# Optimization experiments

Measured on AMD Instinct MI355X. Metric: run time of the kernel, lower is better.

## Reference

```python
import jax, jax.numpy as jnp
import numpy as np

N, E = 50000, 800000
NODE_IN, EDGE_IN, H, L = 2, 2, 128, 3
EPS = 1e-5


def _lin(x, W, b):
    return x @ W + b


def setup_inputs() -> dict:
    key = jax.random.key(0)
    ks = jax.random.split(key, 24)

    def gw(k, shape):
        fan_in = shape[-2]
        return jax.random.uniform(k, shape, jnp.float32, -1.0, 1.0) / np.sqrt(fan_in)

    inp = {
        "x": jax.random.normal(ks[0], (N, NODE_IN), jnp.float32),
        "edge_attr": jax.random.normal(ks[1], (E, EDGE_IN), jnp.float32),
        "edge_index": jax.random.randint(ks[2], (2, E), 0, N, jnp.int32),
        "batch": jnp.zeros((N,), jnp.int32),
        # input MLP: [NODE_IN -> H -> H], Lin+ReLU twice
        "Win0": gw(ks[3], (NODE_IN, H)), "bin0": jnp.zeros((H,), jnp.float32),
        "Win1": gw(ks[4], (H, H)), "bin1": jnp.zeros((H,), jnp.float32),
        # per-layer (stacked over L) IGConv params
        # mlp1: [H+EDGE_IN -> H -> H], Lin+ReLU twice
        "W1a": gw(ks[5], (L, H + EDGE_IN, H)), "b1a": jnp.zeros((L, H), jnp.float32),
        "W1b": gw(ks[6], (L, H, H)), "b1b": jnp.zeros((L, H), jnp.float32),
        # mlp2: [2H -> H] Lin+ReLU, then Lin+Sigmoid [H -> H]
        "W2a": gw(ks[7], (L, 2 * H, H)), "b2a": jnp.zeros((L, H), jnp.float32),
        "W2b": gw(ks[8], (L, H, H)), "b2b": jnp.zeros((L, H), jnp.float32),
        # BatchNorm affine params per layer
        "gamma": jnp.ones((L, H), jnp.float32), "beta": jnp.zeros((L, H), jnp.float32),
        # final MLP: [H -> H] Lin+ReLU, then Lin+Sigmoid [H -> 1]
        "Wf": gw(ks[9], (H, H)), "bf": jnp.zeros((H,), jnp.float32),
        "Wo": gw(ks[10], (H, 1)), "bo": jnp.zeros((1,), jnp.float32),
    }
    return inp


def _forward(x, edge_attr, edge_index, Win0, bin0, Win1, bin1,
             W1a, b1a, W1b, b1b, W2a, b2a, W2b, b2b, gamma, beta, Wf, bf, Wo, bo):
    src, dst = edge_index[0], edge_index[1]  # PyG source->target flow
    n = x.shape[0]

    # input MLP
    h = jax.nn.relu(_lin(x, Win0, bin0))
    h = jax.nn.relu(_lin(h, Win1, bin1))

    # per-edge mean-aggregation denominator (0-degree nodes -> 0 in PyG mean)
    cnt = jax.ops.segment_sum(jnp.ones((src.shape[0],), h.dtype), dst, num_segments=n)
    denom = jnp.maximum(cnt, 1.0)[:, None]  # [N,1]

    for l in range(L):
        # message: mlp1(cat(x_j, edge_attr))
        xj = h[src]                                        # [E,H] gather
        tmp = jnp.concatenate([xj, edge_attr], axis=1)     # [E,H+EDGE_IN]
        m = jax.nn.relu(_lin(tmp, W1a[l], b1a[l]))
        m = jax.nn.relu(_lin(m, W1b[l], b1b[l]))           # [E,H]
        # mean aggregate at targets
        agg = jax.ops.segment_sum(m, dst, num_segments=n) / denom  # [N,H]
        # update: mlp2(cat(x, agg)) -> Lin+ReLU -> Lin+Sigmoid
        u = jnp.concatenate([h, agg], axis=1)
        u = jax.nn.relu(_lin(u, W2a[l], b2a[l]))
        out = jax.nn.sigmoid(_lin(u, W2b[l], b2b[l]))
        # residual + BatchNorm (training-mode batch stats, biased var)
        r = h + out
        mu = jnp.mean(r, axis=0)
        var = jnp.mean((r - mu) ** 2, axis=0)
        h = (r - mu) * jax.lax.rsqrt(var + EPS) * gamma[l] + beta[l]

    # final MLP
    f = jax.nn.relu(_lin(h, Wf, bf))
    return jax.nn.sigmoid(_lin(f, Wo, bo))  # [N,1]


def reference(x, edge_attr, edge_index, batch, Win0, bin0, Win1, bin1,
              W1a, b1a, W1b, b1b, W2a, b2a, W2b, b2b, gamma, beta, Wf, bf, Wo, bo):
    # `batch` is unused by the original forward
    return _forward(x, edge_attr, edge_index, Win0, bin0, Win1, bin1,
                    W1a, b1a, W1b, b1b, W2a, b2a, W2b, b2b, gamma, beta,
                    Wf, bf, Wo, bo)
```

## Files before the change

### kernel.cpp

```cpp
#include <hip/hip_runtime.h>
#include <hip/hip_bf16.h>

#define NN 50000
#define NE 800000
#define HD 128
#define EPSV 1e-5f
#define TE 64
#define BLK 256
#define SROW 68
#define ASTR 336
#define BSTR 272

typedef unsigned short u16;
typedef __attribute__((ext_vector_type(8))) short bf16x8;
typedef __attribute__((ext_vector_type(4))) float f32x4;
#define MFMA16 __builtin_amdgcn_mfma_f32_16x16x32_bf16

__device__ __forceinline__ float sigm(float x){ return 1.0f/(1.0f+__expf(-x)); }
__device__ __forceinline__ void atomAddF(float* p, float v){ unsafeAtomicAdd(p, v); }
__device__ __forceinline__ unsigned bfr(float x){
    unsigned u = __float_as_uint(x);
    return (u + 0x7FFFu + ((u>>16)&1u)) >> 16;
}
__device__ __forceinline__ float bf2f(unsigned u){ return __uint_as_float(u<<16); }

__global__ void zero_i_k(int* __restrict__ p, int n){
    int i = blockIdx.x*blockDim.x + threadIdx.x;
    if (i < n) p[i] = 0;
}

__global__ void zero_agg_bn_k(float4* __restrict__ agg4, int n4, float* __restrict__ bn){
    int i = blockIdx.x*blockDim.x + threadIdx.x;
    if (i < n4) agg4[i] = make_float4(0.f,0.f,0.f,0.f);
    if (i < 256) bn[i] = 0.0f;
}

__global__ void count_k(const int* __restrict__ dst, int* __restrict__ cnt){
    int e = blockIdx.x*blockDim.x + threadIdx.x;
    if (e < NE) atomicAdd(&cnt[dst[e]], 1);
}
__global__ void rdenom_k(const int* __restrict__ cnt, float* __restrict__ rd){
    int i = blockIdx.x*blockDim.x + threadIdx.x;
    if (i < NN) rd[i] = 1.0f / fmaxf((float)cnt[i], 1.0f);
}

__global__ __launch_bounds__(1024) void scan_k(const int* __restrict__ cnt, int* __restrict__ off){
    __shared__ int s[1024];
    __shared__ int carryS;
    const int tid = threadIdx.x;
    if (tid == 0) carryS = 0;
    __syncthreads();
    const int NCH = (NN + 1023) / 1024;
    for (int ch = 0; ch < NCH; ++ch){
        const int i = ch*1024 + tid;
        const int v = (i < NN) ? cnt[i] : 0;
        s[tid] = v;
        __syncthreads();
        #pragma unroll
        for (int ofs = 1; ofs < 1024; ofs <<= 1){
            int t = (tid >= ofs) ? s[tid-ofs] : 0;
            __syncthreads();
            s[tid] += t;
            __syncthreads();
        }
        const int carry = carryS;
        if (i < NN) off[i] = carry + s[tid] - v;
        __syncthreads();
        if (tid == 1023) carryS = carry + s[1023];
        __syncthreads();
    }
    if (tid == 0) off[NN] = NE;
}

__global__ void fill_k(const int* __restrict__ dst, const int* __restrict__ off,
                       int* __restrict__ fill, int* __restrict__ eidx,
                       int* __restrict__ sdst){
    int e = blockIdx.x*blockDim.x + threadIdx.x;
    if (e < NE){
        int d = dst[e];
        int pos = atomicAdd(&fill[d], 1);
        int slot = off[d] + pos;
        eidx[slot] = e;
        sdst[slot] = d;
    }
}

__global__ void wconv_k(const float* __restrict__ src, u16* __restrict__ dst,
                        int K, int KP, int H){
    int idx = blockIdx.x*blockDim.x + threadIdx.x;
    if (idx >= H*KP) return;
    const int l = blockIdx.y;
    src += (size_t)l*K*H;  dst += (size_t)l*H*KP;
    int c = idx / KP, k = idx - c*KP;
    dst[idx] = (k < K) ? (u16)bfr(src[k*H + c]) : (u16)0;
}

__device__ __forceinline__ void mv_acc(const float* sT, int krows,
        const float* __restrict__ W, int c0, int eg, float acc[4][8])
{
    const float* Wp = W + c0;
    #pragma unroll 2
    for (int k=0; k<krows; ++k) {
        const float4 sv = *(const float4*)(sT + k*SROW + eg*4);
        const float4 wa = *(const float4*)(Wp + k*HD);
        const float4 wb = *(const float4*)(Wp + k*HD + 4);
        const float s[4] = {sv.x, sv.y, sv.z, sv.w};
        const float w[8] = {wa.x,wa.y,wa.z,wa.w, wb.x,wb.y,wb.z,wb.w};
        #pragma unroll
        for (int i=0;i<4;++i)
            #pragma unroll
            for (int j=0;j<8;++j)
                acc[i][j] = fmaf(s[i], w[j], acc[i][j]);
    }
}

__device__ __forceinline__ void stage_rows(float* smem, const float* __restrict__ base,
                                           const int* rowsLDS, int tid)
{
    const int e_lo = tid>>3, kq = tid&7;
    #pragma unroll
    for (int half=0; half<2; ++half) {
        const int e = e_lo + 32*half;
        const int row = rowsLDS[e];
        const float* p = base + (size_t)row*HD + kq*4;
        #pragma unroll
        for (int q=0; q<4; ++q) {
            const float4 v = *(const float4*)(p + q*32);
            const int kb = 4*kq + 32*q;
            smem[(kb+0)*SROW + e] = v.x;
            smem[(kb+1)*SROW + e] = v.y;
            smem[(kb+2)*SROW + e] = v.z;
            smem[(kb+3)*SROW + e] = v.w;
        }
    }
}

__global__ __launch_bounds__(BLK) void input_mlp_k(
    const float* __restrict__ x,
    const float* __restrict__ W0, const float* __restrict__ b0,
    const float* __restrict__ W1, const float* __restrict__ b1,
    float* __restrict__ h, u16* __restrict__ hb)
{
    __shared__ float smem[130*SROW];
    const int tid = threadIdx.x;
    const int n0 = blockIdx.x * TE;

    #pragma unroll
    for (int it=0; it<(HD*TE)/BLK; ++it) {
        int task = it*BLK + tid;
        int e = task & (TE-1);
        int c = task >> 6;
        int n = n0 + e; if (n >= NN) n = NN-1;
        float x0 = x[n*2+0], x1 = x[n*2+1];
        smem[c*SROW + e] = fmaxf(fmaf(x0, W0[c], fmaf(x1, W0[HD+c], b0[c])), 0.0f);
    }
    __syncthreads();

    const int cg = tid & 15, eg = tid >> 4, c0 = cg*8;
    float acc[4][8];
    #pragma unroll
    for (int j=0;j<8;++j){ float bv=b1[c0+j];
        #pragma unroll
        for (int i=0;i<4;++i) acc[i][j]=bv; }
    mv_acc(smem, HD, W1, c0, eg, acc);

    #pragma unroll
    for (int i=0;i<4;++i){
        int n = n0 + eg*4 + i;
        if (n < NN) {
            float4 r0, r1;
            r0.x=fmaxf(acc[i][0],0.f); r0.y=fmaxf(acc[i][1],0.f);
            r0.z=fmaxf(acc[i][2],0.f); r0.w=fmaxf(acc[i][3],0.f);
            r1.x=fmaxf(acc[i][4],0.f); r1.y=fmaxf(acc[i][5],0.f);
            r1.z=fmaxf(acc[i][6],0.f); r1.w=fmaxf(acc[i][7],0.f);
            *(float4*)&h[(size_t)n*HD + c0]     = r0;
            *(float4*)&h[(size_t)n*HD + c0 + 4] = r1;
            uint4 pk;
            pk.x = bfr(r0.x)|(bfr(r0.y)<<16); pk.y = bfr(r0.z)|(bfr(r0.w)<<16);
            pk.z = bfr(r1.x)|(bfr(r1.y)<<16); pk.w = bfr(r1.z)|(bfr(r1.w)<<16);
            *(uint4*)&hb[(size_t)n*HD + c0] = pk;
        }
    }
}

__global__ __launch_bounds__(BLK, 4) void edge_msg_kernel(
    const u16* __restrict__ hb, const float* __restrict__ ea,
    const int* __restrict__ src, const int* __restrict__ eidx,
    const int* __restrict__ sdst, const int* __restrict__ off,
    const float* __restrict__ rd,
    const u16* __restrict__ W1aT, const float* __restrict__ b1a,
    const u16* __restrict__ W1bT, const float* __restrict__ b1b,
    float* __restrict__ agg)
{
    __shared__ char bufA[TE*ASTR];
    __shared__ char bufB[TE*BSTR];

    const int tid = threadIdx.x;
    const int lane = tid & 63;
    const int l15 = lane & 15, lhi = lane >> 4;
    const int w = tid >> 6;
    const int s0 = blockIdx.x * TE;
    const int cg = tid & 15, c0 = cg*8;
    const int myrow = tid >> 2, p = tid & 3;
    const int rowL = 16*w + l15;
    const int bl = lane >> 2;

    for (int idx = tid; idx < TE*5; idx += BLK){
        const int r = idx/5, q = idx - r*5;
        *(uint4*)(bufA + r*ASTR + 256 + q*16) = make_uint4(0u,0u,0u,0u);
    }

    {
        const int et  = eidx[s0 + rowL];
        const int sv0 = src[et];
        const int sv  = __shfl(sv0, bl);
        const int etr = __shfl(et,  bl);
        const uint4* sp = (const uint4*)(hb + (size_t)sv*HD);
        uint4* dp = (uint4*)(bufA + myrow*ASTR + p*64);
        #pragma unroll
        for (int q=0;q<4;++q) dp[q] = sp[p*4+q];
        if (p == 0){
            const float2 a = *(const float2*)&ea[(size_t)etr*2];
            *(unsigned*)(bufA + myrow*ASTR + 256) = bfr(a.x) | (bfr(a.y)<<16);
        }
    }
    __syncthreads();

    f32x4 acc1[2][4];
    #pragma unroll
    for (int cc=0; cc<2; ++cc){
        const float4 bv = *(const float4*)&b1a[(2*w+cc)*16 + lhi*4];
        #pragma unroll
        for (int te=0; te<4; ++te){
            acc1[cc][te][0]=bv.x; acc1[cc][te][1]=bv.y;
            acc1[cc][te][2]=bv.z; acc1[cc][te][3]=bv.w;
        }
    }
    #pragma unroll
    for (int kk=0; kk<5; ++kk){
        const bf16x8 a0 = *(const bf16x8*)(W1aT + ((2*w  )*16 + l15)*160 + kk*32 + lhi*8);
        const bf16x8 a1 = *(const bf16x8*)(W1aT + ((2*w+1)*16 + l15)*160 + kk*32 + lhi*8);
        #pragma unroll
        for (int te=0; te<4; ++te){
            const bf16x8 bb = *(const bf16x8*)(bufA + (te*16+l15)*ASTR + kk*64 + lhi*16);
            acc1[0][te] = MFMA16(a0, bb, acc1[0][te], 0,0,0);
            acc1[1][te] = MFMA16(a1, bb, acc1[1][te], 0,0,0);
        }
    }
    #pragma unroll
    for (int cc=0; cc<2; ++cc){
        #pragma unroll
        for (int te=0; te<4; ++te){
            uint2 pk;
            pk.x = bfr(fmaxf(acc1[cc][te][0],0.f)) | (bfr(fmaxf(acc1[cc][te][1],0.f))<<16);
            pk.y = bfr(fmaxf(acc1[cc][te][2],0.f)) | (bfr(fmaxf(acc1[cc][te][3],0.f))<<16);
            *(uint2*)(bufB + (te*16+l15)*BSTR + (2*w+cc)*32 + lhi*8) = pk;
        }
    }
    __syncthreads();

    f32x4 acc2[2][4];
    #pragma unroll
    for (int cc=0; cc<2; ++cc){
        const float4 bv = *(const float4*)&b1b[(2*w+cc)*16 + lhi*4];
        #pragma unroll
        for (int te=0; te<4; ++te){
            acc2[cc][te][0]=bv.x; acc2[cc][te][1]=bv.y;
            acc2[cc][te][2]=bv.z; acc2[cc][te][3]=bv.w;
        }
    }
    #pragma unroll
    for (int kk=0; kk<4; ++kk){
        const bf16x8 a0 = *(const bf16x8*)(W1bT + ((2*w  )*16 + l15)*128 + kk*32 + lhi*8);
        const bf16x8 a1 = *(const bf16x8*)(W1bT + ((2*w+1)*16 + l15)*128 + kk*32 + lhi*8);
        #pragma unroll
        for (int te=0; te<4; ++te){
            const bf16x8 bb = *(const bf16x8*)(bufB + (te*16+l15)*BSTR + kk*64 + lhi*16);
            acc2[0][te] = MFMA16(a0, bb, acc2[0][te], 0,0,0);
            acc2[1][te] = MFMA16(a1, bb, acc2[1][te], 0,0,0);
        }
    }
    __syncthreads();
    #pragma unroll
    for (int cc=0; cc<2; ++cc){
        #pragma unroll
        for (int te=0; te<4; ++te){
            uint2 pk;
            pk.x = bfr(fmaxf(acc2[cc][te][0],0.f)) | (bfr(fmaxf(acc2[cc][te][1],0.f))<<16);
            pk.y = bfr(fmaxf(acc2[cc][te][2],0.f)) | (bfr(fmaxf(acc2[cc][te][3],0.f))<<16);
            *(uint2*)(bufB + (te*16+l15)*BSTR + (2*w+cc)*32 + lhi*8) = pk;
        }
    }
    __syncthreads();

    const int d0 = sdst[s0];
    const int d1 = sdst[s0 + TE - 1];
    const int ng = tid >> 4;
    for (int d = d0 + ng; d <= d1; d += 16){
        const int ob = off[d], oe = off[d+1];
        int lo = ob > s0 ? ob : s0;
        int hi = oe < s0 + TE ? oe : s0 + TE;
        if (lo >= hi) continue;
        float s[8] = {0.f,0.f,0.f,0.f,0.f,0.f,0.f,0.f};
        for (int t = lo; t < hi; ++t){
            const uint4 v = *(const uint4*)(bufB + (t - s0)*BSTR + cg*16);
            s[0] += bf2f(v.x&0xffffu); s[1] += bf2f(v.x>>16);
            s[2] += bf2f(v.y&0xffffu); s[3] += bf2f(v.y>>16);
            s[4] += bf2f(v.z&0xffffu); s[5] += bf2f(v.z>>16);
            s[6] += bf2f(v.w&0xffffu); s[7] += bf2f(v.w>>16);
        }
        const float rdv = rd[d];
        #pragma unroll
        for (int j=0;j<8;++j) s[j] *= rdv;
        float* ap = &agg[(size_t)d*HD + c0];
        if (ob >= s0 && oe <= s0 + TE){
            float4 a0 = make_float4(s[0],s[1],s[2],s[3]);
            float4 a1 = make_float4(s[4],s[5],s[6],s[7]);
            *(float4*)ap = a0; *(float4*)(ap+4) = a1;
        } else {
            #pragma unroll
            for (int j=0;j<8;++j) atomAddF(ap+j, s[j]);
        }
    }
}

__global__ __launch_bounds__(BLK, 4) void node_upd_kernel(
    const float* __restrict__ h, const u16* __restrict__ hb,
    const float* __restrict__ agg,
    const u16* __restrict__ W2aT, const float* __restrict__ b2a,
    const u16* __restrict__ W2bT, const float* __restrict__ b2b,
    float* __restrict__ rbuf)
{
    __shared__ char bufA[TE*ASTR];
    __shared__ char bufB[TE*BSTR];

    const int tid = threadIdx.x;
    const int lane = tid & 63;
    const int l15 = lane & 15, lhi = lane >> 4;
    const int w = tid >> 6;
    const int n0 = blockIdx.x * TE;
    const int myrow = tid >> 2, p = tid & 3;

    {
        int n = n0 + myrow; if (n >= NN) n = NN-1;
        const uint4* sp = (const uint4*)(hb + (size_t)n*HD);
        uint4* dp = (uint4*)(bufA + myrow*ASTR + p*64);
        #pragma unroll
        for (int q=0;q<4;++q) dp[q] = sp[p*4+q];
    }
    __syncthreads();

    f32x4 accN[2][4];
    #pragma unroll
    for (int cc=0; cc<2; ++cc){
        const float4 bv = *(const float4*)&b2a[(2*w+cc)*16 + lhi*4];
        #pragma unroll
        for (int te=0; te<4; ++te){
            accN[cc][te][0]=bv.x; accN[cc][te][1]=bv.y;
            accN[cc][te][2]=bv.z; accN[cc][te][3]=bv.w;
        }
    }
    #pragma unroll
    for (int kk=0; kk<4; ++kk){
        const bf16x8 a0 = *(const bf16x8*)(W2aT + ((2*w  )*16 + l15)*256 + kk*32 + lhi*8);
        const bf16x8 a1 = *(const bf16x8*)(W2aT + ((2*w+1)*16 + l15)*256 + kk*32 + lhi*8);
        #pragma unroll
        for (int te=0; te<4; ++te){
            const bf16x8 bb = *(const bf16x8*)(bufA + (te*16+l15)*ASTR + kk*64 + lhi*16);
            accN[0][te] = MFMA16(a0, bb, accN[0][te], 0,0,0);
            accN[1][te] = MFMA16(a1, bb, accN[1][te], 0,0,0);
        }
    }
    __syncthreads();
    {
        int n = n0 + myrow; if (n >= NN) n = NN-1;
        const float4* sp = (const float4*)(agg + (size_t)n*HD + p*32);
        uint4* dp = (uint4*)(bufA + myrow*ASTR + p*64);
        #pragma unroll
        for (int q=0;q<4;++q){
            const float4 v0 = sp[q*2+0], v1 = sp[q*2+1];
            uint4 pk;
            pk.x = bfr(v0.x)|(bfr(v0.y)<<16); pk.y = bfr(v0.z)|(bfr(v0.w)<<16);
            pk.z = bfr(v1.x)|(bfr(v1.y)<<16); pk.w = bfr(v1.z)|(bfr(v1.w)<<16);
            dp[q] = pk;
        }
    }
    __syncthreads();
    #pragma unroll
    for (int kk=0; kk<4; ++kk){
        const bf16x8 a0 = *(const bf16x8*)(W2aT + ((2*w  )*16 + l15)*256 + 128 + kk*32 + lhi*8);
        const bf16x8 a1 = *(const bf16x8*)(W2aT + ((2*w+1)*16 + l15)*256 + 128 + kk*32 + lhi*8);
        #pragma unroll
        for (int te=0; te<4; ++te){
            const bf16x8 bb = *(const bf16x8*)(bufA + (te*16+l15)*ASTR + kk*64 + lhi*16);
            accN[0][te] = MFMA16(a0, bb, accN[0][te], 0,0,0);
            accN[1][te] = MFMA16(a1, bb, accN[1][te], 0,0,0);
        }
    }
    #pragma unroll
    for (int cc=0; cc<2; ++cc){
        #pragma unroll
        for (int te=0; te<4; ++te){
            uint2 pk;
            pk.x = bfr(fmaxf(accN[cc][te][0],0.f)) | (bfr(fmaxf(accN[cc][te][1],0.f))<<16);
            pk.y = bfr(fmaxf(accN[cc][te][2],0.f)) | (bfr(fmaxf(accN[cc][te][3],0.f))<<16);
            *(uint2*)(bufB + (te*16+l15)*BSTR + (2*w+cc)*32 + lhi*8) = pk;
        }
    }
    __syncthreads();

    f32x4 accO[2][4];
    #pragma unroll
    for (int cc=0; cc<2; ++cc){
        const float4 bv = *(const float4*)&b2b[(2*w+cc)*16 + lhi*4];
        #pragma unroll
        for (int te=0; te<4; ++te){
            accO[cc][te][0]=bv.x; accO[cc][te][1]=bv.y;
            accO[cc][te][2]=bv.z; accO[cc][te][3]=bv.w;
        }
    }
    #pragma unroll
    for (int kk=0; kk<4; ++kk){
        const bf16x8 a0 = *(const bf16x8*)(W2bT + ((2*w  )*16 + l15)*128 + kk*32 + lhi*8);
        const bf16x8 a1 = *(const bf16x8*)(W2bT + ((2*w+1)*16 + l15)*128 + kk*32 + lhi*8);
        #pragma unroll
        for (int te=0; te<4; ++te){
            const bf16x8 bb = *(const bf16x8*)(bufB + (te*16+l15)*BSTR + kk*64 + lhi*16);
            accO[0][te] = MFMA16(a0, bb, accO[0][te], 0,0,0);
            accO[1][te] = MFMA16(a1, bb, accO[1][te], 0,0,0);
        }
    }
    #pragma unroll
    for (int cc=0; cc<2; ++cc){
        const int cbase = (2*w+cc)*16 + lhi*4;
        #pragma unroll
        for (int te=0; te<4; ++te){
            const int n = n0 + te*16 + l15;
            if (n < NN){
                const float4 hv = *(const float4*)&h[(size_t)n*HD + cbase];
                float4 r;
                r.x = hv.x + sigm(accO[cc][te][0]);
                r.y = hv.y + sigm(accO[cc][te][1]);
                r.z = hv.z + sigm(accO[cc][te][2]);
                r.w = hv.w + sigm(accO[cc][te][3]);
                *(float4*)&rbuf[(size_t)n*HD + cbase] = r;
            }
        }
    }
}

__global__ void bn_stats_k(const float* __restrict__ r, float* __restrict__ bn){
    const int c = threadIdx.x & (HD-1);
    const int half = threadIdx.x >> 7;
    const int stride = gridDim.x * 2;
    float s = 0.f, ss = 0.f;
    for (int n = blockIdx.x*2 + half; n < NN; n += stride) {
        const float v = r[(size_t)n*HD + c];
        s += v; ss += v*v;
    }
    atomAddF(&bn[c], s);
    atomAddF(&bn[HD+c], ss);
}

__global__ void bn_norm_k(const float* __restrict__ r, const float* __restrict__ bn,
                          const float* __restrict__ gamma, const float* __restrict__ beta,
                          float* __restrict__ h, u16* __restrict__ hb){
    const int i = blockIdx.x*blockDim.x + threadIdx.x;
    const int n4 = NN*HD/4;
    if (i >= n4) return;
    const int c0 = (i*4) & (HD-1);
    float4 v = ((const float4*)r)[i];
    float* vp = (float*)&v;
    #pragma unroll
    for (int j=0;j<4;++j){
        const int c = c0 + j;
        const float mu  = bn[c] * (1.0f/NN);
        const float var = bn[HD+c] * (1.0f/NN) - mu*mu;
        const float sc  = rsqrtf(var + EPSV) * gamma[c];
        const float sh  = beta[c] - mu*sc;
        vp[j] = fmaf(vp[j], sc, sh);
    }
    ((float4*)h)[i] = v;
    uint2 pk;
    pk.x = bfr(vp[0]) | (bfr(vp[1])<<16);
    pk.y = bfr(vp[2]) | (bfr(vp[3])<<16);
    ((uint2*)hb)[i] = pk;
}

__global__ __launch_bounds__(BLK) void final_kernel(
    const float* __restrict__ h,
    const float* __restrict__ Wf, const float* __restrict__ bf,
    const float* __restrict__ Wo, const float* __restrict__ bo,
    float* __restrict__ out)
{
    __shared__ float smem[130*SROW];
    __shared__ int s_src[TE];
    const int tid = threadIdx.x;
    const int n0 = blockIdx.x * TE;
    const int cg = tid & 15, eg = tid >> 4, c0 = cg*8;

    if (tid < TE) { int n = n0 + tid; s_src[tid] = (n < NN) ? n : NN-1; }
    __syncthreads();
    stage_rows(smem, h, s_src, tid);
    __syncthreads();

    float acc[4][8];
    #pragma unroll
    for (int j=0;j<8;++j){ float bv=bf[c0+j];
        #pragma unroll
        for (int i=0;i<4;++i) acc[i][j]=bv; }
    mv_acc(smem, HD, Wf, c0, eg, acc);
    __syncthreads();

    #pragma unroll
    for (int j=0;j<8;++j){
        float4 m0;
        m0.x=fmaxf(acc[0][j],0.f); m0.y=fmaxf(acc[1][j],0.f);
        m0.z=fmaxf(acc[2][j],0.f); m0.w=fmaxf(acc[3][j],0.f);
        *(float4*)&smem[(c0+j)*SROW + eg*4] = m0;
    }
    __syncthreads();

    const int e = tid >> 2, q = tid & 3;
    float s = 0.f;
    #pragma unroll
    for (int kk=0; kk<32; ++kk) {
        const int k = q*32 + kk;
        s = fmaf(smem[k*SROW + e], Wo[k], s);
    }
    s += __shfl_xor(s, 1);
    s += __shfl_xor(s, 2);
    const int n = n0 + e;
    if (q == 0 && n < NN)
        out[n] = sigm(s + bo[0]);
}

extern "C" void kernel_launch(void* const* d_in, const int* in_sizes, int n_in,
                              void* d_out, int out_size, void* d_ws, size_t ws_size,
                              hipStream_t stream)
{
    const float* x    = (const float*)d_in[0];
    const float* ea   = (const float*)d_in[1];
    const int*   ei   = (const int*)d_in[2];
    const float* Win0 = (const float*)d_in[4];
    const float* bin0 = (const float*)d_in[5];
    const float* Win1 = (const float*)d_in[6];
    const float* bin1 = (const float*)d_in[7];
    const float* W1a  = (const float*)d_in[8];
    const float* b1a  = (const float*)d_in[9];
    const float* W1b  = (const float*)d_in[10];
    const float* b1b  = (const float*)d_in[11];
    const float* W2a  = (const float*)d_in[12];
    const float* b2a  = (const float*)d_in[13];
    const float* W2b  = (const float*)d_in[14];
    const float* b2b  = (const float*)d_in[15];
    const float* gmm  = (const float*)d_in[16];
    const float* bta  = (const float*)d_in[17];
    const float* Wf   = (const float*)d_in[18];
    const float* bfv  = (const float*)d_in[19];
    const float* Wo   = (const float*)d_in[20];
    const float* bo   = (const float*)d_in[21];
    float* out = (float*)d_out;

    char* p = (char*)d_ws;
    float* h     = (float*)p;  p += (size_t)NN*HD*4;
    float* rbuf  = (float*)p;  p += (size_t)NN*HD*4;
    float* agg   = (float*)p;  p += (size_t)NN*HD*4;
    u16*   hb    = (u16*)p;    p += (size_t)NN*HD*2;
    u16*   W1aT  = (u16*)p;    p += (size_t)3*128*160*2;
    u16*   W1bT  = (u16*)p;    p += (size_t)3*128*128*2;
    u16*   W2aT  = (u16*)p;    p += (size_t)3*128*256*2;
    u16*   W2bT  = (u16*)p;    p += (size_t)3*128*128*2;
    float* rd    = (float*)p;  p += (size_t)NN*4;
    float* bn    = (float*)p;  p += 256*4;
    int*   cnt   = (int*)p;    p += (size_t)NN*4;
    int*   fill  = (int*)p;    p += (size_t)NN*4;
    int*   off   = (int*)p;    p += (size_t)(NN+1)*4;
    int*   eidx  = (int*)p;    p += (size_t)NE*4;
    int*   sdst  = (int*)p;

    const int* srcp = ei;
    const int* dstp = ei + NE;

    const int GN = (NN + TE - 1) / TE;
    const int GE = NE / TE;
    const int G4 = (NN*HD/4 + 255) / 256;

    zero_i_k<<<(2*NN+255)/256, 256, 0, stream>>>(cnt, 2*NN);
    count_k<<<(NE+255)/256, 256, 0, stream>>>(dstp, cnt);
    scan_k<<<1, 1024, 0, stream>>>(cnt, off);
    rdenom_k<<<(NN+255)/256, 256, 0, stream>>>(cnt, rd);
    fill_k<<<(NE+255)/256, 256, 0, stream>>>(dstp, off, fill, eidx, sdst);

    wconv_k<<<dim3((128*160+255)/256,3), 256, 0, stream>>>(W1a, W1aT, 130, 160, 128);
    wconv_k<<<dim3((128*128+255)/256,3), 256, 0, stream>>>(W1b, W1bT, 128, 128, 128);
    wconv_k<<<dim3((128*256+255)/256,3), 256, 0, stream>>>(W2a, W2aT, 256, 256, 128);
    wconv_k<<<dim3((128*128+255)/256,3), 256, 0, stream>>>(W2b, W2bT, 128, 128, 128);

    input_mlp_k<<<GN, BLK, 0, stream>>>(x, Win0, bin0, Win1, bin1, h, hb);

    for (int l = 0; l < 3; ++l) {
        zero_agg_bn_k<<<G4, 256, 0, stream>>>((float4*)agg, NN*HD/4, bn);
        edge_msg_kernel<<<GE, BLK, 0, stream>>>(hb, ea, srcp, eidx, sdst, off, rd,
            W1aT + (size_t)l*128*160, b1a + l*HD,
            W1bT + (size_t)l*128*128, b1b + l*HD, agg);
        node_upd_kernel<<<GN, BLK, 0, stream>>>(h, hb, agg,
            W2aT + (size_t)l*128*256, b2a + l*HD,
            W2bT + (size_t)l*128*128, b2b + l*HD, rbuf);
        bn_stats_k<<<400, 256, 0, stream>>>(rbuf, bn);
        bn_norm_k<<<G4, 256, 0, stream>>>(rbuf, bn, gmm + l*HD, bta + l*HD, h, hb);
    }

    final_kernel<<<GN, BLK, 0, stream>>>(h, Wf, bfv, Wo, bo, out);
}
```

Before: 1.165 ms.

## Pre-permute src and edge attrs into CSR order; reuse one LDS buffer

The fill kernel now writes source indices and bf16-packed edge attributes directly in destination-sorted order, so the edge message kernel no longer needs the indirect eidx to src/ea gather on every layer. The second shared-memory buffer is removed and the intermediate activations are written back into bufA, guarded by an extra barrier. Launch bounds are raised from 4 to 7 blocks per SM to exploit the smaller LDS footprint. The trade-offs are higher register pressure from the tighter launch bound and an extra synchronization.

```diff
diff --git a/kernel.cpp b/kernel.cpp
--- a/kernel.cpp
+++ b/kernel.cpp
@@ -72,16 +72,19 @@
     if (tid == 0) off[NN] = NE;
 }
 
-__global__ void fill_k(const int* __restrict__ dst, const int* __restrict__ off,
-                       int* __restrict__ fill, int* __restrict__ eidx,
-                       int* __restrict__ sdst){
+__global__ void fill_k(const int* __restrict__ src, const int* __restrict__ dst,
+                       const float* __restrict__ ea, const int* __restrict__ off,
+                       int* __restrict__ fill, int* __restrict__ ssrc,
+                       unsigned* __restrict__ sea, int* __restrict__ sdst){
     int e = blockIdx.x*blockDim.x + threadIdx.x;
     if (e < NE){
         int d = dst[e];
         int pos = atomicAdd(&fill[d], 1);
         int slot = off[d] + pos;
-        eidx[slot] = e;
+        ssrc[slot] = src[e];
         sdst[slot] = d;
+        const float2 a = *(const float2*)&ea[(size_t)e*2];
+        sea[slot] = bfr(a.x) | (bfr(a.y)<<16);
     }
 }
 
@@ -183,9 +186,9 @@
     }
 }
 
-__global__ __launch_bounds__(BLK, 4) void edge_msg_kernel(
-    const u16* __restrict__ hb, const float* __restrict__ ea,
-    const int* __restrict__ src, const int* __restrict__ eidx,
+__global__ __launch_bounds__(BLK, 7) void edge_msg_kernel(
+    const u16* __restrict__ hb,
+    const int* __restrict__ ssrc, const unsigned* __restrict__ sea,
     const int* __restrict__ sdst, const int* __restrict__ off,
     const float* __restrict__ rd,
     const u16* __restrict__ W1aT, const float* __restrict__ b1a,
@@ -193,7 +196,6 @@
     float* __restrict__ agg)
 {
     __shared__ char bufA[TE*ASTR];
-    __shared__ char bufB[TE*BSTR];
 
     const int tid = threadIdx.x;
     const int lane = tid & 63;
@@ -205,23 +207,24 @@
     const int rowL = 16*w + l15;
     const int bl = lane >> 2;
 
-    for (int idx = tid; idx < TE*5; idx += BLK){
-        const int r = idx/5, q = idx - r*5;
-        *(uint4*)(bufA + r*ASTR + 256 + q*16) = make_uint4(0u,0u,0u,0u);
+    const int d0 = sdst[s0];
+    const int d1 = sdst[s0 + TE - 1];
+
+    for (int idx = tid; idx < TE*4; idx += BLK){
+        const int r = idx >> 2, q = idx & 3;
+        *(uint4*)(bufA + r*ASTR + 272 + q*16) = make_uint4(0u,0u,0u,0u);
     }
 
     {
-        const int et  = eidx[s0 + rowL];
-        const int sv0 = src[et];
+        const int sv0 = ssrc[s0 + rowL];
         const int sv  = __shfl(sv0, bl);
-        const int etr = __shfl(et,  bl);
         const uint4* sp = (const uint4*)(hb + (size_t)sv*HD);
         uint4* dp = (uint4*)(bufA + myrow*ASTR + p*64);
         #pragma unroll
         for (int q=0;q<4;++q) dp[q] = sp[p*4+q];
         if (p == 0){
-            const float2 a = *(const float2*)&ea[(size_t)etr*2];
-            *(unsigned*)(bufA + myrow*ASTR + 256) = bfr(a.x) | (bfr(a.y)<<16);
+            const unsigned eaw = sea[s0 + myrow];
+            *(uint4*)(bufA + myrow*ASTR + 256) = make_uint4(eaw, 0u, 0u, 0u);
         }
     }
     __syncthreads();
@@ -247,6 +250,7 @@
             acc1[1][te] = MFMA16(a1, bb, acc1[1][te], 0,0,0);
         }
     }
+    __syncthreads();
     #pragma unroll
     for (int cc=0; cc<2; ++cc){
         #pragma unroll
@@ -254,7 +258,7 @@
             uint2 pk;
             pk.x = bfr(fmaxf(acc1[cc][te][0],0.f)) | (bfr(fmaxf(acc1[cc][te][1],0.f))<<16);
             pk.y = bfr(fmaxf(acc1[cc][te][2],0.f)) | (bfr(fmaxf(acc1[cc][te][3],0.f))<<16);
-            *(uint2*)(bufB + (te*16+l15)*BSTR + (2*w+cc)*32 + lhi*8) = pk;
+            *(uint2*)(bufA + (te*16+l15)*ASTR + (2*w+cc)*32 + lhi*8) = pk;
         }
     }
     __syncthreads();
@@ -275,7 +279,7 @@
         const bf16x8 a1 = *(const bf16x8*)(W1bT + ((2*w+1)*16 + l15)*128 + kk*32 + lhi*8);
         #pragma unroll
         for (int te=0; te<4; ++te){
-            const bf16x8 bb = *(const bf16x8*)(bufB + (te*16+l15)*BSTR + kk*64 + lhi*16);
+            const bf16x8 bb = *(const bf16x8*)(bufA + (te*16+l15)*ASTR + kk*64 + lhi*16);
             acc2[0][te] = MFMA16(a0, bb, acc2[0][te], 0,0,0);
             acc2[1][te] = MFMA16(a1, bb, acc2[1][te], 0,0,0);
         }
@@ -288,13 +292,11 @@
             uint2 pk;
             pk.x = bfr(fmaxf(acc2[cc][te][0],0.f)) | (bfr(fmaxf(acc2[cc][te][1],0.f))<<16);
             pk.y = bfr(fmaxf(acc2[cc][te][2],0.f)) | (bfr(fmaxf(acc2[cc][te][3],0.f))<<16);
-            *(uint2*)(bufB + (te*16+l15)*BSTR + (2*w+cc)*32 + lhi*8) = pk;
-        }
-    }
-    __syncthreads();
-
-    const int d0 = sdst[s0];
-    const int d1 = sdst[s0 + TE - 1];
+            *(uint2*)(bufA + (te*16+l15)*ASTR + (2*w+cc)*32 + lhi*8) = pk;
+        }
+    }
+    __syncthreads();
+
     const int ng = tid >> 4;
     for (int d = d0 + ng; d <= d1; d += 16){
         const int ob = off[d], oe = off[d+1];
@@ -303,7 +305,7 @@
         if (lo >= hi) continue;
         float s[8] = {0.f,0.f,0.f,0.f,0.f,0.f,0.f,0.f};
         for (int t = lo; t < hi; ++t){
-            const uint4 v = *(const uint4*)(bufB + (t - s0)*BSTR + cg*16);
+            const uint4 v = *(const uint4*)(bufA + (t - s0)*ASTR + cg*16);
             s[0] += bf2f(v.x&0xffffu); s[1] += bf2f(v.x>>16);
             s[2] += bf2f(v.y&0xffffu); s[3] += bf2f(v.y>>16);
             s[4] += bf2f(v.z&0xffffu); s[5] += bf2f(v.z>>16);
@@ -576,8 +578,9 @@
     int*   cnt   = (int*)p;    p += (size_t)NN*4;
     int*   fill  = (int*)p;    p += (size_t)NN*4;
     int*   off   = (int*)p;    p += (size_t)(NN+1)*4;
-    int*   eidx  = (int*)p;    p += (size_t)NE*4;
-    int*   sdst  = (int*)p;
+    int*   ssrc  = (int*)p;    p += (size_t)NE*4;
+    int*   sdst  = (int*)p;    p += (size_t)NE*4;
+    unsigned* sea = (unsigned*)p;
 
     const int* srcp = ei;
     const int* dstp = ei + NE;
@@ -590,7 +593,7 @@
     count_k<<<(NE+255)/256, 256, 0, stream>>>(dstp, cnt);
     scan_k<<<1, 1024, 0, stream>>>(cnt, off);
     rdenom_k<<<(NN+255)/256, 256, 0, stream>>>(cnt, rd);
-    fill_k<<<(NE+255)/256, 256, 0, stream>>>(dstp, off, fill, eidx, sdst);
+    fill_k<<<(NE+255)/256, 256, 0, stream>>>(srcp, dstp, ea, off, fill, ssrc, sea, sdst);
 
     wconv_k<<<dim3((128*160+255)/256,3), 256, 0, stream>>>(W1a, W1aT, 130, 160, 128);
     wconv_k<<<dim3((128*128+255)/256,3), 256, 0, stream>>>(W1b, W1bT, 128, 128, 128);
@@ -601,7 +604,7 @@
 
     for (int l = 0; l < 3; ++l) {
         zero_agg_bn_k<<<G4, 256, 0, stream>>>((float4*)agg, NN*HD/4, bn);
-        edge_msg_kernel<<<GE, BLK, 0, stream>>>(hb, ea, srcp, eidx, sdst, off, rd,
+        edge_msg_kernel<<<GE, BLK, 0, stream>>>(hb, ssrc, sea, sdst, off, rd,
             W1aT + (size_t)l*128*160, b1a + l*HD,
             W1bT + (size_t)l*128*128, b1b + l*HD, agg);
         node_upd_kernel<<<GN, BLK, 0, stream>>>(h, hb, agg,
```

Result: faster. 1.048 ms (-10.0%).
